# Optimization experiments

Measured on AMD Instinct MI355X. Metric: run time of the kernel, lower is better.

The kernel has to match this reference:

```python
import jax, jax.numpy as jnp
from jax import lax
import numpy as np

B, T, K = 256, 512, 256
MAX_SEQ = 512  # max_sequence_length; output padded to MAX_SEQ + 2


def setup_inputs() -> dict:
    key = jax.random.key(0)
    k1, k2 = jax.random.split(key)
    emissions = jax.random.normal(k1, (B, T, K), dtype=jnp.float32)
    transitions = jax.random.normal(k2, (K, K), dtype=jnp.float32)
    mask = jnp.ones((B, T), dtype=jnp.int32)  # prefix mask; here full-length
    return {"emissions": emissions, "transitions": transitions, "mask": mask,
            "max_sequence_length": MAX_SEQ}


def _crf_decode(emissions, transitions, mask):
    # emissions: [B, T, K] float; transitions: [K, K]; mask: [B, T] int (prefix 1s)
    b, t, k = emissions.shape
    state0 = emissions[:, 0, :]                      # [B, K]
    em_rest = jnp.swapaxes(emissions[:, 1:, :], 0, 1)  # [T-1, B, K]
    mk_rest = jnp.swapaxes(mask[:, 1:], 0, 1)           # [T-1, B]

    def fwd(state, xs):
        em_t, mk_t = xs
        # scores[b, i, j] = state[b, i] + transitions[i, j]  (prev tag i -> cur tag j)
        scores = state[:, :, None] + transitions[None, :, :]   # [B, K, K]
        bp = jnp.argmax(scores, axis=1).astype(jnp.int32)       # [B, K] best prev tag
        new_state = jnp.max(scores, axis=1) + em_t              # [B, K]
        valid = (mk_t > 0)[:, None]
        # RNN-with-mask semantics: keep last valid state past sequence end
        return jnp.where(valid, new_state, state), bp

    last_state, bps = lax.scan(fwd, state0, (em_rest, mk_rest))  # bps: [T-1, B, K]
    last_tag = jnp.argmax(last_state, axis=-1).astype(jnp.int32)  # [B]

    def bwd(tag, xs):
        bp_t, mk_t = xs
        out = tag  # tag at this timestep
        prev = jnp.take_along_axis(bp_t, tag[:, None], axis=1)[:, 0]
        tag = jnp.where(mk_t > 0, prev, tag)  # only step back on valid positions
        return tag, out

    tag0, outs = lax.scan(bwd, last_tag, (bps, mk_rest), reverse=True)
    # outs[t] = tag at position t+1 (t = 0..T-2); tag0 = tag at position 0
    tags = jnp.concatenate([tag0[:, None], jnp.swapaxes(outs, 0, 1)], axis=1)  # [B, T]
    return tags


def reference(emissions, transitions, mask, max_sequence_length):
    tags = _crf_decode(emissions, transitions, mask)
    tags = tags * mask  # zero out padding positions
    pad = max_sequence_length + 2 - tags.shape[1]
    return jnp.pad(tags, ((0, 0), (0, pad)))
```

## Files before the change

kernel.cpp:

```cpp
#include <hip/hip_runtime.h>


#define TK 256
#define TT 512

__global__ void transpose_kernel(const float* __restrict__ trans,
                                 float* __restrict__ transT) {
  int j = blockIdx.x;
  int i = threadIdx.x;
  transT[(size_t)j * TK + i] = trans[(size_t)i * TK + j];
}

__global__ __launch_bounds__(512, 2) void crf_fwd(const float* __restrict__ em,
                                                  const float* __restrict__ trans,
                                                  const int* __restrict__ mask,
                                                  float* __restrict__ states) {
  const int b = blockIdx.x;
  const int tid = threadIdx.x;
  const int j = tid & (TK - 1);
  const int h = tid >> 8;

  __shared__ __align__(16) float st[TK];
  __shared__ float part[TK];
  __shared__ int mk[TT];

  float tr[128];
#pragma unroll
  for (int i = 0; i < 128; ++i)
    tr[i] = trans[(size_t)(h * 128 + i) * TK + j];

  mk[tid] = mask[(size_t)b * TT + tid];

  const size_t base = (size_t)b * TT * TK;
  if (h == 0) {
    float s0 = em[base + j];
    st[j] = s0;
    states[base + j] = s0;
  }
  __syncthreads();

  const float* stp = st + h * 128;
  for (int t = 1; t < TT; ++t) {
    float emv = 0.f;
    if (h == 0) emv = em[base + (size_t)t * TK + j];

    float m0 = -INFINITY, m1 = -INFINITY;
#pragma unroll
    for (int k = 0; k < 32; ++k) {
      const float4 s4 = *reinterpret_cast<const float4*>(stp + 4 * k);
      float a0 = s4.x + tr[4 * k + 0];
      float a1 = s4.y + tr[4 * k + 1];
      float a2 = s4.z + tr[4 * k + 2];
      float a3 = s4.w + tr[4 * k + 3];
      m0 = fmaxf(fmaxf(m0, a0), a1);
      m1 = fmaxf(fmaxf(m1, a2), a3);
    }
    float m = fmaxf(m0, m1);
    if (h == 1) part[j] = m;
    __syncthreads();
    if (h == 0) {
      m = fmaxf(m, part[j]);
      float nv = (mk[t] > 0) ? (m + emv) : st[j];
      st[j] = nv;
      states[base + (size_t)t * TK + j] = nv;
    }
    __syncthreads();
  }
}

__device__ __forceinline__ float wave_max(float m) {
#pragma unroll
  for (int d = 1; d < 64; d <<= 1) m = fmaxf(m, __shfl_xor(m, d, 64));
  return m;
}

__device__ __forceinline__ int first_eq_idx(float s0, float s1, float s2,
                                            float s3, float m) {
  unsigned long long b0 = __ballot(s0 == m);
  unsigned long long b1 = __ballot(s1 == m);
  unsigned long long b2 = __ballot(s2 == m);
  unsigned long long b3 = __ballot(s3 == m);
  int best = 0x7fffffff;
  if (b0) best = min(best, 4 * (__ffsll(b0) - 1) + 0);
  if (b1) best = min(best, 4 * (__ffsll(b1) - 1) + 1);
  if (b2) best = min(best, 4 * (__ffsll(b2) - 1) + 2);
  if (b3) best = min(best, 4 * (__ffsll(b3) - 1) + 3);
  return best;
}

__global__ __launch_bounds__(64, 1) void crf_bwd(const float* __restrict__ states,
                                                 const float* __restrict__ transT,
                                                 const int* __restrict__ mask,
                                                 int* __restrict__ out,
                                                 int out_stride) {
  const int b = blockIdx.x;
  const int lane = threadIdx.x;

  __shared__ int mk[TT];
  for (int q = lane; q < TT; q += 64) mk[q] = mask[(size_t)b * TT + q];
  __syncthreads();

  const size_t sbase = (size_t)b * TT * TK;
  int* outp = out + (size_t)b * out_stride;

  for (int q = TT + lane; q < out_stride; q += 64) outp[q] = 0;

  const float* srow = states + sbase;
  float4 r = *reinterpret_cast<const float4*>(srow + (size_t)(TT - 1) * TK + 4 * lane);
  float lm = fmaxf(fmaxf(r.x, r.y), fmaxf(r.z, r.w));
  lm = wave_max(lm);
  int tag = first_eq_idx(r.x, r.y, r.z, r.w, lm);

  auto LOADROW = [&](int rr) -> float4 {
    return *reinterpret_cast<const float4*>(srow + (size_t)rr * TK + 4 * lane);
  };
  float4 p0 = LOADROW(TT - 2), p1 = LOADROW(TT - 3), p2 = LOADROW(TT - 4),
         p3 = LOADROW(TT - 5);

  auto STEP = [&](float4 pr, int t) {
    int mkt = mk[t];
    if (lane == 0) outp[t] = (mkt > 0) ? tag : 0;
    const float4 tv =
        *reinterpret_cast<const float4*>(transT + (size_t)tag * TK + 4 * lane);
    float s0 = pr.x + tv.x;
    float s1 = pr.y + tv.y;
    float s2 = pr.z + tv.z;
    float s3 = pr.w + tv.w;
    float m = fmaxf(fmaxf(s0, s1), fmaxf(s2, s3));
    m = wave_max(m);
    int prev = first_eq_idx(s0, s1, s2, s3, m);
    tag = (mkt > 0) ? prev : tag;
  };

  int t = TT - 1;
  while (t >= 4) {
    STEP(p0, t);     if (t - 5 >= 0) p0 = LOADROW(t - 5);
    STEP(p1, t - 1); if (t - 6 >= 0) p1 = LOADROW(t - 6);
    STEP(p2, t - 2); if (t - 7 >= 0) p2 = LOADROW(t - 7);
    STEP(p3, t - 3); if (t - 8 >= 0) p3 = LOADROW(t - 8);
    t -= 4;
  }
  STEP(p0, 3);
  STEP(p1, 2);
  STEP(p2, 1);
  if (lane == 0) outp[0] = (mk[0] > 0) ? tag : 0;
}

extern "C" void kernel_launch(void* const* d_in, const int* in_sizes, int n_in,
                              void* d_out, int out_size, void* d_ws, size_t ws_size,
                              hipStream_t stream) {
  const float* em = (const float*)d_in[0];
  const float* trans = (const float*)d_in[1];
  const int* mask = (const int*)d_in[2];
  int* out = (int*)d_out;

  const int B = in_sizes[0] / (TT * TK);
  const int out_stride = out_size / B;

  float* states = (float*)d_ws;
  float* transT = states + (size_t)B * TT * TK;

  transpose_kernel<<<TK, TK, 0, stream>>>(trans, transT);
  crf_fwd<<<B, 512, 0, stream>>>(em, trans, mask, states);
  crf_bwd<<<B, 64, 0, stream>>>(states, transT, mask, out, out_stride);
}
```

Baseline: 746.4 us.

## Split forward max-reduction across four thread groups of 1024-thread blocks

```diff
diff --git a/kernel.cpp b/kernel.cpp
--- a/kernel.cpp
+++ b/kernel.cpp
@@ -3,6 +3,8 @@
 
 #define TK 256
 #define TT 512
+
+typedef float v2f __attribute__((ext_vector_type(2)));
 
 __global__ void transpose_kernel(const float* __restrict__ trans,
                                  float* __restrict__ transT) {
@@ -11,58 +13,69 @@
   transT[(size_t)j * TK + i] = trans[(size_t)i * TK + j];
 }
 
-__global__ __launch_bounds__(512, 2) void crf_fwd(const float* __restrict__ em,
-                                                  const float* __restrict__ trans,
-                                                  const int* __restrict__ mask,
-                                                  float* __restrict__ states) {
+__global__ __launch_bounds__(1024, 4) void crf_fwd(const float* __restrict__ em,
+                                                   const float* __restrict__ trans,
+                                                   const int* __restrict__ mask,
+                                                   float* __restrict__ states) {
   const int b = blockIdx.x;
   const int tid = threadIdx.x;
   const int j = tid & (TK - 1);
   const int h = tid >> 8;
 
   __shared__ __align__(16) float st[TK];
-  __shared__ float part[TK];
+  __shared__ float part[3 * TK];
   __shared__ int mk[TT];
 
-  float tr[128];
+  v2f tr2[32];
 #pragma unroll
-  for (int i = 0; i < 128; ++i)
-    tr[i] = trans[(size_t)(h * 128 + i) * TK + j];
+  for (int i = 0; i < 32; ++i) {
+    tr2[i].x = trans[(size_t)(h * 64 + 2 * i + 0) * TK + j];
+    tr2[i].y = trans[(size_t)(h * 64 + 2 * i + 1) * TK + j];
+  }
 
-  mk[tid] = mask[(size_t)b * TT + tid];
+  if (tid < TT) mk[tid] = mask[(size_t)b * TT + tid];
 
   const size_t base = (size_t)b * TT * TK;
+  float cur = 0.f;
   if (h == 0) {
-    float s0 = em[base + j];
-    st[j] = s0;
-    states[base + j] = s0;
+    cur = em[base + j];
+    st[j] = cur;
+    states[base + j] = cur;
   }
   __syncthreads();
 
-  const float* stp = st + h * 128;
+  const float* stp = st + h * 64;
+  const float* emp = em + base + TK + j;
+  float* outp = states + base + TK + j;
+
   for (int t = 1; t < TT; ++t) {
     float emv = 0.f;
-    if (h == 0) emv = em[base + (size_t)t * TK + j];
+    if (h == 0) emv = *emp;
 
     float m0 = -INFINITY, m1 = -INFINITY;
 #pragma unroll
-    for (int k = 0; k < 32; ++k) {
+    for (int k = 0; k < 16; ++k) {
       const float4 s4 = *reinterpret_cast<const float4*>(stp + 4 * k);
-      float a0 = s4.x + tr[4 * k + 0];
-      float a1 = s4.y + tr[4 * k + 1];
-      float a2 = s4.z + tr[4 * k + 2];
-      float a3 = s4.w + tr[4 * k + 3];
-      m0 = fmaxf(fmaxf(m0, a0), a1);
-      m1 = fmaxf(fmaxf(m1, a2), a3);
+      v2f a = {s4.x, s4.y};
+      v2f c = {s4.z, s4.w};
+      a = a + tr2[2 * k + 0];
+      c = c + tr2[2 * k + 1];
+      m0 = fmaxf(fmaxf(m0, a.x), a.y);
+      m1 = fmaxf(fmaxf(m1, c.x), c.y);
     }
-    float m = fmaxf(m0, m1);
-    if (h == 1) part[j] = m;
+    const float pm = fmaxf(m0, m1);
+
+    if (h) part[(h - 1) * TK + j] = pm;
     __syncthreads();
     if (h == 0) {
-      m = fmaxf(m, part[j]);
-      float nv = (mk[t] > 0) ? (m + emv) : st[j];
+      float m = fmaxf(fmaxf(pm, part[j]),
+                      fmaxf(part[TK + j], part[2 * TK + j]));
+      float nv = (mk[t] > 0) ? (m + emv) : cur;
+      cur = nv;
       st[j] = nv;
-      states[base + (size_t)t * TK + j] = nv;
+      *outp = nv;
+      emp += TK;
+      outp += TK;
     }
     __syncthreads();
   }
@@ -161,6 +174,6 @@
   float* transT = states + (size_t)B * TT * TK;
 
   transpose_kernel<<<TK, TK, 0, stream>>>(trans, transT);
-  crf_fwd<<<B, 512, 0, stream>>>(em, trans, mask, states);
+  crf_fwd<<<B, 1024, 0, stream>>>(em, trans, mask, states);
   crf_bwd<<<B, 64, 0, stream>>>(states, transT, mask, out, out_stride);
 }
```

Result: faster. 655.9 us (-12.1%).

## Split forward max-plus over 16 waves with LDS partials and shuffle reduction

Applied to the files above, without the earlier changes.

```diff
diff --git a/kernel.cpp b/kernel.cpp
--- a/kernel.cpp
+++ b/kernel.cpp
@@ -3,6 +3,14 @@
 
 #define TK 256
 #define TT 512
+
+typedef float v4f __attribute__((ext_vector_type(4)));
+
+__device__ __forceinline__ float max3f(float a, float b, float c) {
+  float d;
+  asm("v_max3_f32 %0, %1, %2, %3" : "=v"(d) : "v"(a), "v"(b), "v"(c));
+  return d;
+}
 
 __global__ void transpose_kernel(const float* __restrict__ trans,
                                  float* __restrict__ transT) {
@@ -11,58 +19,101 @@
   transT[(size_t)j * TK + i] = trans[(size_t)i * TK + j];
 }
 
-__global__ __launch_bounds__(512, 2) void crf_fwd(const float* __restrict__ em,
-                                                  const float* __restrict__ trans,
-                                                  const int* __restrict__ mask,
-                                                  float* __restrict__ states) {
+__global__ __launch_bounds__(1024)
+__attribute__((amdgpu_waves_per_eu(4, 4)))
+void crf_fwd(const float* __restrict__ em,
+             const float* __restrict__ trans,
+             const int* __restrict__ mask,
+             float* __restrict__ states) {
   const int b = blockIdx.x;
   const int tid = threadIdx.x;
-  const int j = tid & (TK - 1);
-  const int h = tid >> 8;
-
-  __shared__ __align__(16) float st[TK];
-  __shared__ float part[TK];
+  const int lane = tid & 63;
+  const int g = tid >> 6;
+  const int c = lane & 3;
+  const int j0 = 4 * lane;
+  const int fj = 16 * g + 4 * c;
+
+  __shared__ __align__(16) float st[2][TK];
+  __shared__ __align__(16) v4f part[16][64];
   __shared__ int mk[TT];
 
-  float tr[128];
-#pragma unroll
-  for (int i = 0; i < 128; ++i)
-    tr[i] = trans[(size_t)(h * 128 + i) * TK + j];
-
-  mk[tid] = mask[(size_t)b * TT + tid];
+  const float* tb = trans + (size_t)(16 * g) * TK + j0;
+#define TRD(n) const v4f t##n = *reinterpret_cast<const v4f*>(tb + (n) * TK);
+  TRD(0) TRD(1) TRD(2) TRD(3) TRD(4) TRD(5) TRD(6) TRD(7)
+  TRD(8) TRD(9) TRD(10) TRD(11) TRD(12) TRD(13) TRD(14) TRD(15)
+#undef TRD
+
+  if (tid < TT) mk[tid] = mask[(size_t)b * TT + tid];
 
   const size_t base = (size_t)b * TT * TK;
-  if (h == 0) {
-    float s0 = em[base + j];
-    st[j] = s0;
-    states[base + j] = s0;
+  if (lane < 4) {
+    const v4f s0 = *reinterpret_cast<const v4f*>(em + base + 16 * g + 4 * lane);
+    *reinterpret_cast<v4f*>(&st[0][16 * g + 4 * lane]) = s0;
+    *reinterpret_cast<v4f*>(states + base + 16 * g + 4 * lane) = s0;
   }
   __syncthreads();
 
-  const float* stp = st + h * 128;
+  const float* emf = em + base + fj;
+  float* stg = states + base + 16 * g + 4 * lane;
+
   for (int t = 1; t < TT; ++t) {
-    float emv = 0.f;
-    if (h == 0) emv = em[base + (size_t)t * TK + j];
-
-    float m0 = -INFINITY, m1 = -INFINITY;
+    const int rd = (t - 1) & 1, wr = t & 1;
+    const v4f emv = *reinterpret_cast<const v4f*>(emf + (size_t)t * TK);
+    const int mkt = mk[t];
+    const v4f OS = *reinterpret_cast<const v4f*>(&st[rd][fj]);
+
+    const float* sp = &st[rd][16 * g];
+    const v4f S0 = *reinterpret_cast<const v4f*>(sp);
+    const v4f S1 = *reinterpret_cast<const v4f*>(sp + 4);
+    const v4f S2 = *reinterpret_cast<const v4f*>(sp + 8);
+    const v4f S3 = *reinterpret_cast<const v4f*>(sp + 12);
+
+    v4f acc;
+    {
+      const v4f a0 = t0 + S0.x;
+      const v4f b0 = t1 + S0.y;
+      acc.x = fmaxf(a0.x, b0.x);
+      acc.y = fmaxf(a0.y, b0.y);
+      acc.z = fmaxf(a0.z, b0.z);
+      acc.w = fmaxf(a0.w, b0.w);
+    }
+#define ROWPAIR(tA, tB, sA, sB)            \
+    {                                      \
+      const v4f aa = tA + sA;              \
+      const v4f bb = tB + sB;              \
+      acc.x = max3f(acc.x, aa.x, bb.x);    \
+      acc.y = max3f(acc.y, aa.y, bb.y);    \
+      acc.z = max3f(acc.z, aa.z, bb.z);    \
+      acc.w = max3f(acc.w, aa.w, bb.w);    \
+    }
+    ROWPAIR(t2, t3, S0.z, S0.w)
+    ROWPAIR(t4, t5, S1.x, S1.y)
+    ROWPAIR(t6, t7, S1.z, S1.w)
+    ROWPAIR(t8, t9, S2.x, S2.y)
+    ROWPAIR(t10, t11, S2.z, S2.w)
+    ROWPAIR(t12, t13, S3.x, S3.y)
+    ROWPAIR(t14, t15, S3.z, S3.w)
+#undef ROWPAIR
+
+    part[g][lane] = acc;
+    __syncthreads();
+
+    v4f P = part[lane >> 2][4 * g + c];
 #pragma unroll
-    for (int k = 0; k < 32; ++k) {
-      const float4 s4 = *reinterpret_cast<const float4*>(stp + 4 * k);
-      float a0 = s4.x + tr[4 * k + 0];
-      float a1 = s4.y + tr[4 * k + 1];
-      float a2 = s4.z + tr[4 * k + 2];
-      float a3 = s4.w + tr[4 * k + 3];
-      m0 = fmaxf(fmaxf(m0, a0), a1);
-      m1 = fmaxf(fmaxf(m1, a2), a3);
-    }
-    float m = fmaxf(m0, m1);
-    if (h == 1) part[j] = m;
-    __syncthreads();
-    if (h == 0) {
-      m = fmaxf(m, part[j]);
-      float nv = (mk[t] > 0) ? (m + emv) : st[j];
-      st[j] = nv;
-      states[base + (size_t)t * TK + j] = nv;
+    for (int m = 4; m <= 32; m <<= 1) {
+      P.x = fmaxf(P.x, __shfl_xor(P.x, m, 64));
+      P.y = fmaxf(P.y, __shfl_xor(P.y, m, 64));
+      P.z = fmaxf(P.z, __shfl_xor(P.z, m, 64));
+      P.w = fmaxf(P.w, __shfl_xor(P.w, m, 64));
+    }
+    v4f nw;
+    nw.x = (mkt > 0) ? P.x + emv.x : OS.x;
+    nw.y = (mkt > 0) ? P.y + emv.y : OS.y;
+    nw.z = (mkt > 0) ? P.z + emv.z : OS.z;
+    nw.w = (mkt > 0) ? P.w + emv.w : OS.w;
+    if (lane < 4) {
+      *reinterpret_cast<v4f*>(&st[wr][16 * g + 4 * lane]) = nw;
+      *reinterpret_cast<v4f*>(stg + (size_t)t * TK) = nw;
     }
     __syncthreads();
   }
@@ -161,6 +212,6 @@
   float* transT = states + (size_t)B * TT * TK;
 
   transpose_kernel<<<TK, TK, 0, stream>>>(trans, transT);
-  crf_fwd<<<B, 512, 0, stream>>>(em, trans, mask, states);
+  crf_fwd<<<B, 1024, 0, stream>>>(em, trans, mask, states);
   crf_bwd<<<B, 64, 0, stream>>>(states, transT, mask, out, out_stride);
 }
```

After: 1.191 ms. +59.6%, slower.

## Restructure CRF forward pass across 16 waves with packed adds and one barrier

Applied to the files above, without the earlier changes.

```diff
diff --git a/kernel.cpp b/kernel.cpp
--- a/kernel.cpp
+++ b/kernel.cpp
@@ -3,6 +3,20 @@
 
 #define TK 256
 #define TT 512
+
+typedef float v2f __attribute__((ext_vector_type(2)));
+
+__device__ __forceinline__ float max3f(float a, float b, float c) {
+  float d;
+  asm("v_max3_f32 %0, %1, %2, %3" : "=v"(d) : "v"(a), "v"(b), "v"(c));
+  return d;
+}
+
+__device__ __forceinline__ v2f pk_add(v2f a, v2f b) {
+  v2f d;
+  asm("v_pk_add_f32 %0, %1, %2" : "=v"(d) : "v"(a), "v"(b));
+  return d;
+}
 
 __global__ void transpose_kernel(const float* __restrict__ trans,
                                  float* __restrict__ transT) {
@@ -11,60 +25,89 @@
   transT[(size_t)j * TK + i] = trans[(size_t)i * TK + j];
 }
 
-__global__ __launch_bounds__(512, 2) void crf_fwd(const float* __restrict__ em,
-                                                  const float* __restrict__ trans,
-                                                  const int* __restrict__ mask,
-                                                  float* __restrict__ states) {
+#define K16(X) X(0) X(1) X(2) X(3) X(4) X(5) X(6) X(7) \
+               X(8) X(9) X(10) X(11) X(12) X(13) X(14) X(15)
+
+__global__ __launch_bounds__(1024)
+__attribute__((amdgpu_waves_per_eu(4, 4)))
+void crf_fwd(const float* __restrict__ em,
+             const float* __restrict__ transT,
+             const int* __restrict__ mask,
+             float* __restrict__ states) {
   const int b = blockIdx.x;
   const int tid = threadIdx.x;
-  const int j = tid & (TK - 1);
-  const int h = tid >> 8;
-
-  __shared__ __align__(16) float st[TK];
-  __shared__ float part[TK];
+  const int lane = tid & 63;
+  const int w = tid >> 6;
+  const int g = w >> 1;
+  const int p = w & 1;
+  const int j0 = 128 * p + 2 * lane;
+  const int jm = 32 * g + (lane >> 1);
+
+  __shared__ __align__(16) float st_w[16][32];
+  __shared__ __align__(16) float part[2][8][TK];
   __shared__ int mk[TT];
 
-  float tr[128];
-#pragma unroll
-  for (int i = 0; i < 128; ++i)
-    tr[i] = trans[(size_t)(h * 128 + i) * TK + j];
-
-  mk[tid] = mask[(size_t)b * TT + tid];
+  const float* ta = transT + (size_t)j0 * TK + 32 * g;
+  const float* tb = ta + TK;
+#define TRD(n) \
+  const v2f TA##n = *reinterpret_cast<const v2f*>(ta + 2 * (n)); \
+  const v2f TB##n = *reinterpret_cast<const v2f*>(tb + 2 * (n));
+  K16(TRD)
+#undef TRD
+
+  if (tid < TT) mk[tid] = mask[(size_t)b * TT + tid];
 
   const size_t base = (size_t)b * TT * TK;
-  if (h == 0) {
-    float s0 = em[base + j];
-    st[j] = s0;
-    states[base + j] = s0;
+  float ns = em[base + jm];
+  if ((lane & 1) == 0) {
+    st_w[w][lane >> 1] = ns;
+    if (p == 0) states[base + jm] = ns;
   }
+  float em_n1 = em[base + TK + jm];
+  float em_n2 = em[base + 2 * TK + jm];
   __syncthreads();
 
-  const float* stp = st + h * 128;
+  const float* stw = st_w[w];
+
   for (int t = 1; t < TT; ++t) {
-    float emv = 0.f;
-    if (h == 0) emv = em[base + (size_t)t * TK + j];
-
-    float m0 = -INFINITY, m1 = -INFINITY;
-#pragma unroll
-    for (int k = 0; k < 32; ++k) {
-      const float4 s4 = *reinterpret_cast<const float4*>(stp + 4 * k);
-      float a0 = s4.x + tr[4 * k + 0];
-      float a1 = s4.y + tr[4 * k + 1];
-      float a2 = s4.z + tr[4 * k + 2];
-      float a3 = s4.w + tr[4 * k + 3];
-      m0 = fmaxf(fmaxf(m0, a0), a1);
-      m1 = fmaxf(fmaxf(m1, a2), a3);
+    const float em_cur = em_n1;
+    em_n1 = em_n2;
+    if (t + 2 < TT) em_n2 = em[base + (size_t)(t + 2) * TK + jm];
+
+    v2f a0, b0;
+    {
+      const v2f SP = *reinterpret_cast<const v2f*>(stw);
+      a0 = pk_add(TA0, SP);
+      b0 = pk_add(TB0, SP);
     }
-    float m = fmaxf(m0, m1);
-    if (h == 1) part[j] = m;
+    float accx = fmaxf(a0.x, a0.y);
+    float accy = fmaxf(b0.x, b0.y);
+#define ROWK(n)                                                   \
+    if ((n) > 0) {                                                \
+      const v2f SP = *reinterpret_cast<const v2f*>(stw + 2 * (n));\
+      const v2f aa = pk_add(TA##n, SP);                           \
+      const v2f bb = pk_add(TB##n, SP);                           \
+      accx = max3f(accx, aa.x, aa.y);                             \
+      accy = max3f(accy, bb.x, bb.y);                             \
+    }
+    K16(ROWK)
+#undef ROWK
+
+    *reinterpret_cast<v2f*>(&part[t & 1][g][j0]) = (v2f){accx, accy};
     __syncthreads();
-    if (h == 0) {
-      m = fmaxf(m, part[j]);
-      float nv = (mk[t] > 0) ? (m + emv) : st[j];
-      st[j] = nv;
-      states[base + (size_t)t * TK + j] = nv;
+
+    const float* pb = &part[t & 1][4 * (lane & 1)][jm];
+    const float v0 = pb[0];
+    const float v1 = pb[TK];
+    const float v2 = pb[2 * TK];
+    const float v3 = pb[3 * TK];
+    const float f = fmaxf(max3f(v0, v1, v2), v3);
+    const float m = fmaxf(f, __shfl_xor(f, 1, 64));
+    ns = (mk[t] > 0) ? (m + em_cur) : ns;
+    if ((lane & 1) == 0) {
+      st_w[w][lane >> 1] = ns;
+      if (p == 0) states[base + (size_t)t * TK + jm] = ns;
     }
-    __syncthreads();
   }
 }
 
@@ -161,6 +204,6 @@
   float* transT = states + (size_t)B * TT * TK;
 
   transpose_kernel<<<TK, TK, 0, stream>>>(trans, transT);
-  crf_fwd<<<B, 512, 0, stream>>>(em, trans, mask, states);
+  crf_fwd<<<B, 1024, 0, stream>>>(em, transT, mask, states);
   crf_bwd<<<B, 64, 0, stream>>>(states, transT, mask, out, out_stride);
 }
```

New measurement: 768.7 us. +3.0%, slower.
